# Kernel tuning notes

Hardware: AMD Instinct MI355X
Metric: run time of the kernel (lower is better)

The kernel has to match this reference:

```python
import jax, jax.numpy as jnp
import numpy as np


def _make_grid(h, w, stride=1):
    """Vectorized port of gen_grid_coordinates_exp. Returns (1, 3*Ho, 3*Wo, 2) float32,
    last dim = (x_norm, y_norm) in [-1,1] (torch grid_sample convention)."""
    rows = np.arange(0, h, stride)
    cols = np.arange(0, w, stride)
    theta = -((rows + 0.5) / h * np.pi - np.pi / 2)          # (Ho,)
    phi = (cols + 0.5) / w * 2 * np.pi - np.pi               # (Wo,)
    dtheta = np.pi / h
    dphi = 2 * np.pi / w
    # 3x3 tangent-plane offsets (du: horizontal, dv: vertical), per get_exp_duv
    du = np.tan(dphi) * np.array([[-1., 0., 1.]] * 3)                      # (3,3)
    dv = np.tan(dtheta) * np.array([[1., 1., 1.], [0., 0., 0.], [-1., -1., -1.]])
    T = theta[:, None, None, None]   # (Ho,1,1,1)
    P = phi[None, :, None, None]     # (1,Wo,1,1)
    u_x = -du * np.sin(P) - dv * np.sin(T) * np.cos(P)       # (Ho,Wo,3,3)
    u_y = du * np.cos(P) - dv * np.sin(T) * np.sin(P)
    u_z = dv * np.cos(T) + np.zeros_like(u_x)
    u_norm = np.sqrt(u_x ** 2 + u_y ** 2 + u_z ** 2)
    u_div = np.where(u_norm == 0, 1.0, u_norm)
    c, s = np.cos(u_norm), np.sin(u_norm)
    ex = np.cos(T) * np.cos(P) * c + u_x / u_div * s
    ey = np.cos(T) * np.sin(P) * c + u_y / u_div * s
    ez = np.sin(T) * c + u_z / u_div * s
    new_phi = np.arctan2(ey, ex)
    new_theta = np.arcsin(np.clip(ez, -1.0, 1.0))
    new_r = (-new_theta + np.pi / 2) * h / np.pi - 0.5
    new_c = ((new_phi + np.pi) * w / (2 * np.pi) - 0.5 + w) % w
    # kernel center samples the original integer pixel exactly
    new_r[:, :, 1, 1] = rows[:, None]
    new_c[:, :, 1, 1] = cols[None, :]
    gx = new_c * 2.0 / w - 1.0
    gy = new_r * 2.0 / h - 1.0
    grid = np.stack([gx, gy], axis=-1)                        # (Ho,Wo,3,3,2)
    Ho, Wo = len(rows), len(cols)
    grid = grid.transpose(0, 2, 1, 3, 4).reshape(1, Ho * 3, Wo * 3, 2)
    return grid.astype(np.float32)


def _grid_sample_bilinear(x, grid):
    """torch.nn.functional.grid_sample(mode='bilinear', padding='zeros', align_corners=False).
    x: (B,C,H,W); grid: (1,Hg,Wg,2) shared across batch."""
    B, C, H, W = x.shape
    gx = grid[0, ..., 0]
    gy = grid[0, ..., 1]
    Hg, Wg = gx.shape
    ix = ((gx + 1.0) * W - 1.0) * 0.5   # unnormalize, align_corners=False
    iy = ((gy + 1.0) * H - 1.0) * 0.5
    x0 = jnp.floor(ix); x1 = x0 + 1.0
    y0 = jnp.floor(iy); y1 = y0 + 1.0
    xf = x.reshape(B, C, H * W)

    def corner(xc, yc, wgt):
        valid = (xc >= 0) & (xc < W) & (yc >= 0) & (yc < H)
        xi = jnp.clip(xc, 0, W - 1).astype(jnp.int32)
        yi = jnp.clip(yc, 0, H - 1).astype(jnp.int32)
        idx = (yi * W + xi).reshape(-1)                      # (Hg*Wg,)
        w_eff = (wgt * valid.astype(wgt.dtype)).reshape(-1)  # zero-pad OOB
        return xf[:, :, idx] * w_eff                          # (B,C,Hg*Wg)

    out = (corner(x0, y0, (x1 - ix) * (y1 - iy))
           + corner(x1, y0, (ix - x0) * (y1 - iy))
           + corner(x0, y1, (x1 - ix) * (iy - y0))
           + corner(x1, y1, (ix - x0) * (iy - y0)))
    return out.reshape(B, C, Hg, Wg)


def setup_inputs() -> dict:
    key = jax.random.key(0)
    k1, k2 = jax.random.split(key)
    B, Cin, Cout, H, W = 4, 128, 256, 128, 256
    x = jax.random.normal(k1, (B, Cin, H, W), dtype=jnp.float32)
    # kaiming_uniform_(a=sqrt(5)) -> U(-1/sqrt(fan_in), 1/sqrt(fan_in)), fan_in = Cin*9
    bound = 1.0 / np.sqrt(Cin * 9)
    weight = jax.random.uniform(k2, (Cout, Cin, 3, 3), dtype=jnp.float32,
                                minval=-bound, maxval=bound)
    bias = jnp.zeros((Cout,), dtype=jnp.float32)
    grid = jnp.asarray(_make_grid(H, W, stride=1))  # (1, 3H, 3W, 2)
    return {"x": x, "weight": weight, "bias": bias, "grid": grid}


def reference(x, weight, bias, grid):
    sampled = _grid_sample_bilinear(x, grid)                 # (B,C,3H,3W)
    out = jax.lax.conv_general_dilated(
        sampled, weight, window_strides=(3, 3), padding='VALID',
        dimension_numbers=('NCHW', 'OIHW', 'NCHW'))          # (B,Cout,H,W)
    return out + bias[None, :, None, None]
```

## Files before the change

kernel.cpp:

```cpp
#include <hip/hip_runtime.h>


#define Hh   128
#define Ww   256
#define HWp  (Hh*Ww)
#define CIN  128
#define COUT 256
#define KTOT 1152
#define NPTS (384*768)
#define BM   64
#define BN   256
#define BK   32
#define NKS  (KTOT/BK)

typedef __attribute__((ext_vector_type(8))) __bf16 bf16x8;
typedef __attribute__((ext_vector_type(4))) __bf16 bf16x4;
typedef __attribute__((ext_vector_type(4))) float  f32x4;

__global__ void prep(const float* __restrict__ grid, const float* __restrict__ w,
                     int2* __restrict__ tI, float4* __restrict__ tW,
                     __bf16* __restrict__ wt) {
    if (blockIdx.x < NPTS / 256) {
        int g = blockIdx.x * 256 + threadIdx.x;
        int hh = g / 768, ww = g - hh * 768;
        int ho = hh / 3, ii = hh - 3 * ho;
        int wo = ww / 3, jj = ww - 3 * wo;

        float gx = grid[2 * g + 0];
        float gy = grid[2 * g + 1];
        float ix = ((gx + 1.0f) * (float)Ww - 1.0f) * 0.5f;
        float iy = ((gy + 1.0f) * (float)Hh - 1.0f) * 0.5f;
        float x0f = floorf(ix), y0f = floorf(iy);
        int x0 = (int)x0f, y0 = (int)y0f;
        float wx1 = ix - x0f, wx0 = 1.0f - wx1;
        float wy1 = iy - y0f, wy0 = 1.0f - wy1;

        float wyt = (y0 >= 0 && y0 < Hh) ? wy0 : 0.0f;
        float wyb = (y0 + 1 >= 0 && y0 + 1 < Hh) ? wy1 : 0.0f;
        int r0 = min(max(y0, 0), Hh - 1);
        int r1 = min(max(y0 + 1, 0), Hh - 1);

        int xb; float cw0, cw1;
        if (x0 < 0)            { xb = 0;      cw0 = wx1; cw1 = 0.0f; }
        else if (x0 > Ww - 2)  { xb = Ww - 2; cw0 = 0.0f; cw1 = wx0; }
        else                   { xb = x0;     cw0 = wx0; cw1 = wx1; }

        int e = (ho * Ww + wo) * 9 + ii * 3 + jj;
        tI[e] = make_int2(r0 * Ww + xb, r1 * Ww + xb);
        tW[e] = make_float4(cw0 * wyt, cw1 * wyt, cw0 * wyb, cw1 * wyb);
    } else {
        int o = (blockIdx.x - NPTS / 256) * 256 + threadIdx.x;
        int kk = o & (BK - 1);
        int n  = (o >> 5) & (COUT - 1);
        int ks = o >> 13;
        int ij = ks % 9;
        int ci = (ks / 9) * 32 + kk;
        wt[o] = (__bf16)w[n * KTOT + ci * 9 + ij];
    }
}

__global__ __launch_bounds__(512, 4) void sphconv_gemm(
    const float* __restrict__ x, const __bf16* __restrict__ wt,
    const float* __restrict__ bias, const int2* __restrict__ tI,
    const float4* __restrict__ tW, float* __restrict__ out) {

    __shared__ int2   sTI[BM * 9];
    __shared__ float4 sTW[BM * 9];
    __shared__ __align__(16) __bf16 sA[2][BM * 40];
    __shared__ __align__(16) __bf16 sB[2][BN * 40];

    const int t   = threadIdx.x;
    const int m0  = blockIdx.x * BM;
    const int b   = m0 >> 15;
    const int sp0 = m0 & (HWp - 1);
    const float* xb_ = x + (size_t)b * (CIN * HWp);

    for (int e = t; e < BM * 9; e += 512) {
        sTI[e] = tI[sp0 * 9 + e];
        sTW[e] = tW[sp0 * 9 + e];
    }

    const int lane = t & 63;
    const int wid  = t >> 6;
    const int wrow = wid >> 2;
    const int wcol = wid & 3;
    const int quad = lane >> 4;
    const int l16  = lane & 15;

    const int mr_s = t & 63;
    const int kg   = t >> 6;
    const int wn   = t >> 1;
    const int wkq  = (t & 1) * 16;

    f32x4 acc[2][4];
#pragma unroll
    for (int r = 0; r < 2; ++r)
#pragma unroll
        for (int c = 0; c < 4; ++c) {
            f32x4 z = {0.0f, 0.0f, 0.0f, 0.0f};
            acc[r][c] = z;
        }

    __syncthreads();

    {
        const int2   o  = sTI[mr_s * 9 + 0];
        const float4 wv = sTW[mr_s * 9 + 0];
        const float* img = xb_ + (size_t)(kg * 4) * HWp;
        bf16x4 av;
#pragma unroll
        for (int j = 0; j < 4; ++j) {
            float2 p0 = *(const float2*)(img + o.x);
            float2 p1 = *(const float2*)(img + o.y);
            av[j] = (__bf16)(p0.x * wv.x + p0.y * wv.y + p1.x * wv.z + p1.y * wv.w);
            img += HWp;
        }
        *(bf16x4*)(&sA[0][mr_s * 40 + kg * 4]) = av;
        const __bf16* src = wt + t * 16;
        *(bf16x8*)(&sB[0][wn * 40 + wkq])     = *(const bf16x8*)(src);
        *(bf16x8*)(&sB[0][wn * 40 + wkq + 8]) = *(const bf16x8*)(src + 8);
    }
    __syncthreads();

    int ij = 0, cb = 0;
    for (int ks = 0; ks < NKS; ++ks) {
        const int cur = ks & 1, nxt = cur ^ 1;

        float2 qx[4], qy[4];
        bf16x8 pb0, pb1;
        float4 wv2;
        const bool have = (ks + 1 < NKS);
        int ij2 = (ij == 8) ? 0 : ij + 1;
        int cb2 = (ij == 8) ? cb + 32 : cb;
        if (have) {
            const int2 o = sTI[mr_s * 9 + ij2];
            wv2 = sTW[mr_s * 9 + ij2];
            const float* img = xb_ + (size_t)(cb2 + kg * 4) * HWp;
#pragma unroll
            for (int j = 0; j < 4; ++j) {
                qx[j] = *(const float2*)(img + o.x);
                qy[j] = *(const float2*)(img + o.y);
                img += HWp;
            }
            const __bf16* src = wt + (ks + 1) * (COUT * BK) + t * 16;
            pb0 = *(const bf16x8*)(src);
            pb1 = *(const bf16x8*)(src + 8);
        }

        bf16x8 af[2], bfr[4];
#pragma unroll
        for (int r = 0; r < 2; ++r)
            af[r] = *(const bf16x8*)(&sA[cur][(wrow * 32 + r * 16 + l16) * 40 + quad * 8]);
#pragma unroll
        for (int c = 0; c < 4; ++c)
            bfr[c] = *(const bf16x8*)(&sB[cur][(wcol * 64 + c * 16 + l16) * 40 + quad * 8]);
#pragma unroll
        for (int r = 0; r < 2; ++r)
#pragma unroll
            for (int c = 0; c < 4; ++c)
                acc[r][c] = __builtin_amdgcn_mfma_f32_16x16x32_bf16(
                    af[r], bfr[c], acc[r][c], 0, 0, 0);

        if (have) {
            bf16x4 av;
#pragma unroll
            for (int j = 0; j < 4; ++j)
                av[j] = (__bf16)(qx[j].x * wv2.x + qx[j].y * wv2.y +
                                 qy[j].x * wv2.z + qy[j].y * wv2.w);
            *(bf16x4*)(&sA[nxt][mr_s * 40 + kg * 4]) = av;
            *(bf16x8*)(&sB[nxt][wn * 40 + wkq])     = pb0;
            *(bf16x8*)(&sB[nxt][wn * 40 + wkq + 8]) = pb1;
        }

        __syncthreads();
        ij = ij2; cb = cb2;
    }

#pragma unroll
    for (int c = 0; c < 4; ++c) {
        int n = wcol * 64 + c * 16 + l16;
        float bv = bias[n];
        float* outn = out + (((size_t)(b * COUT + n)) << 15) + sp0;
#pragma unroll
        for (int r = 0; r < 2; ++r) {
            int mbase = wrow * 32 + r * 16 + quad * 4;
            float4 v = make_float4(acc[r][c][0] + bv, acc[r][c][1] + bv,
                                   acc[r][c][2] + bv, acc[r][c][3] + bv);
            *(float4*)(&outn[mbase]) = v;
        }
    }
}

extern "C" void kernel_launch(void* const* d_in, const int* in_sizes, int n_in,
                              void* d_out, int out_size, void* d_ws, size_t ws_size,
                              hipStream_t stream) {
    const float* x    = (const float*)d_in[0];
    const float* w    = (const float*)d_in[1];
    const float* bias = (const float*)d_in[2];
    const float* grid = (const float*)d_in[3];
    float* out = (float*)d_out;

    char* ws = (char*)d_ws;
    int2*   tI = (int2*)(ws);
    float4* tW = (float4*)(ws + 2359296);
    __bf16* wt = (__bf16*)(ws + 7077888);

    prep<<<NPTS / 256 + (NKS * COUT * BK) / 256, 256, 0, stream>>>(grid, w, tI, tW, wt);
    sphconv_gemm<<<(4 * HWp) / BM, 512, 0, stream>>>(x, wt, bias, tI, tW, out);
}
```

Baseline: 396.4 us.

## Pre-transpose input to channel-last fp16 and vectorize bilinear gather in GEMM

Adds a prep stage that converts x from NCHW fp32 into an NHWC fp16 copy, so each A-tile thread gathers 8 contiguous channels per corner with 16-byte loads instead of strided per-channel fp32 loads. The work is specialised: half the threads build the A tile with packed fp16 bilinear math and half load the B tile. The kernel switches from bf16 to fp16 MFMA and swizzles the block order across batches. This trades an extra pass over x and more workspace for far fewer, coalesced gather loads. The packed fp16 interpolation may also change numerics slightly.

```diff
diff --git a/kernel.cpp b/kernel.cpp
--- a/kernel.cpp
+++ b/kernel.cpp
@@ -13,15 +13,25 @@
 #define BK   32
 #define NKS  (KTOT/BK)
 
-typedef __attribute__((ext_vector_type(8))) __bf16 bf16x8;
-typedef __attribute__((ext_vector_type(4))) __bf16 bf16x4;
-typedef __attribute__((ext_vector_type(4))) float  f32x4;
+typedef __attribute__((ext_vector_type(8))) _Float16 f16x8;
+typedef __attribute__((ext_vector_type(4))) float    f32x4;
+
+__device__ __forceinline__ f16x8 bcast8(float f) {
+    _Float16 h = (_Float16)f;
+    f16x8 v;
+#pragma unroll
+    for (int i = 0; i < 8; ++i) v[i] = h;
+    return v;
+}
 
 __global__ void prep(const float* __restrict__ grid, const float* __restrict__ w,
+                     const float* __restrict__ x,
                      int2* __restrict__ tI, float4* __restrict__ tW,
-                     __bf16* __restrict__ wt) {
-    if (blockIdx.x < NPTS / 256) {
-        int g = blockIdx.x * 256 + threadIdx.x;
+                     _Float16* __restrict__ wt2, _Float16* __restrict__ xt) {
+    const int bid = blockIdx.x;
+    const int t   = threadIdx.x;
+    if (bid < NPTS / 256) {
+        int g = bid * 256 + t;
         int hh = g / 768, ww = g - hh * 768;
         int ho = hh / 3, ii = hh - 3 * ho;
         int wo = ww / 3, jj = ww - 3 * wo;
@@ -48,36 +58,49 @@
         int e = (ho * Ww + wo) * 9 + ii * 3 + jj;
         tI[e] = make_int2(r0 * Ww + xb, r1 * Ww + xb);
         tW[e] = make_float4(cw0 * wyt, cw1 * wyt, cw0 * wyb, cw1 * wyb);
-    } else {
-        int o = (blockIdx.x - NPTS / 256) * 256 + threadIdx.x;
+    } else if (bid < 2 * (NPTS / 256)) {
+        int o = (bid - NPTS / 256) * 256 + t;
         int kk = o & (BK - 1);
         int n  = (o >> 5) & (COUT - 1);
         int ks = o >> 13;
         int ij = ks % 9;
         int ci = (ks / 9) * 32 + kk;
-        wt[o] = (__bf16)w[n * KTOT + ci * 9 + ij];
+        wt2[o] = (_Float16)w[n * KTOT + ci * 9 + ij];
+    } else {
+        int r  = (bid - 2 * (NPTS / 256)) * 256 + t;
+        int sp = r & (HWp - 1);
+        int cg = (r >> 15) & 15;
+        int b  = r >> 19;
+        const float* src = x + ((size_t)(b * CIN + cg * 8)) * HWp + sp;
+        f16x8 v;
+#pragma unroll
+        for (int j = 0; j < 8; ++j) v[j] = (_Float16)src[(size_t)j * HWp];
+        *(f16x8*)&xt[((size_t)(b * HWp + sp)) * CIN + cg * 8] = v;
     }
 }
 
 __global__ __launch_bounds__(512, 4) void sphconv_gemm(
-    const float* __restrict__ x, const __bf16* __restrict__ wt,
+    const _Float16* __restrict__ xt, const _Float16* __restrict__ wt2,
     const float* __restrict__ bias, const int2* __restrict__ tI,
     const float4* __restrict__ tW, float* __restrict__ out) {
 
-    __shared__ int2   sTI[BM * 9];
-    __shared__ float4 sTW[BM * 9];
-    __shared__ __align__(16) __bf16 sA[2][BM * 40];
-    __shared__ __align__(16) __bf16 sB[2][BN * 40];
-
-    const int t   = threadIdx.x;
-    const int m0  = blockIdx.x * BM;
+    __shared__ int2   sTI[9 * BM];
+    __shared__ float4 sTW[9 * BM];
+    __shared__ __align__(16) _Float16 sA[2][BM * 40];
+    __shared__ __align__(16) _Float16 sB[2][BN * 40];
+
+    const int t = threadIdx.x;
+    const int bid = blockIdx.x;
+    const int swz = (bid & 7) * 256 + (bid >> 3);
+    const int m0  = swz * BM;
     const int b   = m0 >> 15;
     const int sp0 = m0 & (HWp - 1);
-    const float* xb_ = x + (size_t)b * (CIN * HWp);
-
-    for (int e = t; e < BM * 9; e += 512) {
-        sTI[e] = tI[sp0 * 9 + e];
-        sTW[e] = tW[sp0 * 9 + e];
+    const _Float16* xb_ = xt + (size_t)b * (HWp * CIN);
+
+    for (int e = t; e < 9 * BM; e += 512) {
+        int r = e & (BM - 1), ij = e >> 6;
+        sTI[e] = tI[(sp0 + r) * 9 + ij];
+        sTW[e] = tW[(sp0 + r) * 9 + ij];
     }
 
     const int lane = t & 63;
@@ -87,10 +110,10 @@
     const int quad = lane >> 4;
     const int l16  = lane & 15;
 
-    const int mr_s = t & 63;
-    const int kg   = t >> 6;
-    const int wn   = t >> 1;
-    const int wkq  = (t & 1) * 16;
+    const bool isA = (t < 256);
+    const int  mr  = t & 63;
+    const int  chb = ((t >> 6) & 3) * 8;
+    const int  u   = t - 256;
 
     f32x4 acc[2][4];
 #pragma unroll
@@ -103,73 +126,77 @@
 
     __syncthreads();
 
-    {
-        const int2   o  = sTI[mr_s * 9 + 0];
-        const float4 wv = sTW[mr_s * 9 + 0];
-        const float* img = xb_ + (size_t)(kg * 4) * HWp;
-        bf16x4 av;
-#pragma unroll
-        for (int j = 0; j < 4; ++j) {
-            float2 p0 = *(const float2*)(img + o.x);
-            float2 p1 = *(const float2*)(img + o.y);
-            av[j] = (__bf16)(p0.x * wv.x + p0.y * wv.y + p1.x * wv.z + p1.y * wv.w);
-            img += HWp;
-        }
-        *(bf16x4*)(&sA[0][mr_s * 40 + kg * 4]) = av;
-        const __bf16* src = wt + t * 16;
-        *(bf16x8*)(&sB[0][wn * 40 + wkq])     = *(const bf16x8*)(src);
-        *(bf16x8*)(&sB[0][wn * 40 + wkq + 8]) = *(const bf16x8*)(src + 8);
+    f16x8 p00, p01, p10, p11;
+    float4 wv;
+    f16x8 b0v, b1v, b2v, b3v;
+    if (isA) {
+        const int2 o = sTI[mr];
+        wv = sTW[mr];
+        const _Float16* p = xb_ + (size_t)o.x * CIN + chb;
+        const _Float16* q = xb_ + (size_t)o.y * CIN + chb;
+        p00 = *(const f16x8*)p;  p01 = *(const f16x8*)(p + CIN);
+        p10 = *(const f16x8*)q;  p11 = *(const f16x8*)(q + CIN);
+        f16x8 av = p00 * bcast8(wv.x) + p01 * bcast8(wv.y)
+                 + p10 * bcast8(wv.z) + p11 * bcast8(wv.w);
+        *(f16x8*)&sA[0][mr * 40 + chb] = av;
+    } else {
+        const _Float16* src = wt2 + u * BK;
+        b0v = *(const f16x8*)(src);      b1v = *(const f16x8*)(src + 8);
+        b2v = *(const f16x8*)(src + 16); b3v = *(const f16x8*)(src + 24);
+        *(f16x8*)&sB[0][u * 40 + 0]  = b0v;
+        *(f16x8*)&sB[0][u * 40 + 8]  = b1v;
+        *(f16x8*)&sB[0][u * 40 + 16] = b2v;
+        *(f16x8*)&sB[0][u * 40 + 24] = b3v;
     }
     __syncthreads();
 
     int ij = 0, cb = 0;
     for (int ks = 0; ks < NKS; ++ks) {
         const int cur = ks & 1, nxt = cur ^ 1;
-
-        float2 qx[4], qy[4];
-        bf16x8 pb0, pb1;
-        float4 wv2;
         const bool have = (ks + 1 < NKS);
-        int ij2 = (ij == 8) ? 0 : ij + 1;
-        int cb2 = (ij == 8) ? cb + 32 : cb;
+        const int ij2 = (ij == 8) ? 0 : ij + 1;
+        const int cb2 = (ij == 8) ? cb + 32 : cb;
+
         if (have) {
-            const int2 o = sTI[mr_s * 9 + ij2];
-            wv2 = sTW[mr_s * 9 + ij2];
-            const float* img = xb_ + (size_t)(cb2 + kg * 4) * HWp;
-#pragma unroll
-            for (int j = 0; j < 4; ++j) {
-                qx[j] = *(const float2*)(img + o.x);
-                qy[j] = *(const float2*)(img + o.y);
-                img += HWp;
+            if (isA) {
+                const int2 o = sTI[ij2 * BM + mr];
+                wv = sTW[ij2 * BM + mr];
+                const _Float16* p = xb_ + (size_t)o.x * CIN + cb2 + chb;
+                const _Float16* q = xb_ + (size_t)o.y * CIN + cb2 + chb;
+                p00 = *(const f16x8*)p;  p01 = *(const f16x8*)(p + CIN);
+                p10 = *(const f16x8*)q;  p11 = *(const f16x8*)(q + CIN);
+            } else {
+                const _Float16* src = wt2 + (size_t)(ks + 1) * (COUT * BK) + u * BK;
+                b0v = *(const f16x8*)(src);      b1v = *(const f16x8*)(src + 8);
+                b2v = *(const f16x8*)(src + 16); b3v = *(const f16x8*)(src + 24);
             }
-            const __bf16* src = wt + (ks + 1) * (COUT * BK) + t * 16;
-            pb0 = *(const bf16x8*)(src);
-            pb1 = *(const bf16x8*)(src + 8);
-        }
-
-        bf16x8 af[2], bfr[4];
+        }
+
+        f16x8 af[2], bfr[4];
 #pragma unroll
         for (int r = 0; r < 2; ++r)
-            af[r] = *(const bf16x8*)(&sA[cur][(wrow * 32 + r * 16 + l16) * 40 + quad * 8]);
+            af[r] = *(const f16x8*)(&sA[cur][(wrow * 32 + r * 16 + l16) * 40 + quad * 8]);
 #pragma unroll
         for (int c = 0; c < 4; ++c)
-            bfr[c] = *(const bf16x8*)(&sB[cur][(wcol * 64 + c * 16 + l16) * 40 + quad * 8]);
+            bfr[c] = *(const f16x8*)(&sB[cur][(wcol * 64 + c * 16 + l16) * 40 + quad * 8]);
 #pragma unroll
         for (int r = 0; r < 2; ++r)
 #pragma unroll
             for (int c = 0; c < 4; ++c)
-                acc[r][c] = __builtin_amdgcn_mfma_f32_16x16x32_bf16(
+                acc[r][c] = __builtin_amdgcn_mfma_f32_16x16x32_f16(
                     af[r], bfr[c], acc[r][c], 0, 0, 0);
 
         if (have) {
-            bf16x4 av;
-#pragma unroll
-            for (int j = 0; j < 4; ++j)
-                av[j] = (__bf16)(qx[j].x * wv2.x + qx[j].y * wv2.y +
-                                 qy[j].x * wv2.z + qy[j].y * wv2.w);
-            *(bf16x4*)(&sA[nxt][mr_s * 40 + kg * 4]) = av;
-            *(bf16x8*)(&sB[nxt][wn * 40 + wkq])     = pb0;
-            *(bf16x8*)(&sB[nxt][wn * 40 + wkq + 8]) = pb1;
+            if (isA) {
+                f16x8 av = p00 * bcast8(wv.x) + p01 * bcast8(wv.y)
+                         + p10 * bcast8(wv.z) + p11 * bcast8(wv.w);
+                *(f16x8*)&sA[nxt][mr * 40 + chb] = av;
+            } else {
+                *(f16x8*)&sB[nxt][u * 40 + 0]  = b0v;
+                *(f16x8*)&sB[nxt][u * 40 + 8]  = b1v;
+                *(f16x8*)&sB[nxt][u * 40 + 16] = b2v;
+                *(f16x8*)&sB[nxt][u * 40 + 24] = b3v;
+            }
         }
 
         __syncthreads();
@@ -201,10 +228,11 @@
     float* out = (float*)d_out;
 
     char* ws = (char*)d_ws;
-    int2*   tI = (int2*)(ws);
-    float4* tW = (float4*)(ws + 2359296);
-    __bf16* wt = (__bf16*)(ws + 7077888);
-
-    prep<<<NPTS / 256 + (NKS * COUT * BK) / 256, 256, 0, stream>>>(grid, w, tI, tW, wt);
-    sphconv_gemm<<<(4 * HWp) / BM, 512, 0, stream>>>(x, wt, bias, tI, tW, out);
-}
+    int2*     tI  = (int2*)(ws);
+    float4*   tW  = (float4*)(ws + 2359296);
+    _Float16* wt2 = (_Float16*)(ws + 7077888);
+    _Float16* xt  = (_Float16*)(ws + 7667712);
+
+    prep<<<1152 + 1152 + 8192, 256, 0, stream>>>(grid, w, x, tI, tW, wt2, xt);
+    sphconv_gemm<<<(4 * HWp) / BM, 512, 0, stream>>>(xt, wt2, bias, tI, tW, out);
+}
```

After: 416.5 us. 1.05x slower.
